# Kernel tuning notes

Measured on AMD Instinct MI355X. Metric: run time of the kernel, lower is better.

Reference implementation:

```python
import jax, jax.numpy as jnp
import numpy as np

N, F_IN, HEADS, D_HEAD, HID, OUT, E = 50000, 128, 4, 64, 256, 2, 800000
NEG_SLOPE = 0.2


def setup_inputs() -> dict:
    key = jax.random.key(0)
    ks = jax.random.split(key, 12)
    x = jax.random.normal(ks[0], (N, F_IN), dtype=jnp.float32)
    edge_index = jax.random.randint(ks[1], (2, E), 0, N, dtype=jnp.int64)
    s = 0.05
    W_gat = jax.random.normal(ks[2], (F_IN, HEADS * D_HEAD), dtype=jnp.float32) * s
    att_src = jax.random.normal(ks[3], (HEADS, D_HEAD), dtype=jnp.float32) * s
    att_dst = jax.random.normal(ks[4], (HEADS, D_HEAD), dtype=jnp.float32) * s
    b_gat = jnp.zeros((HEADS * D_HEAD,), dtype=jnp.float32)
    W1 = jax.random.normal(ks[5], (HEADS * D_HEAD, HID), dtype=jnp.float32) * s
    b1 = jnp.zeros((HID,), dtype=jnp.float32)
    W2 = jax.random.normal(ks[6], (HID, HID), dtype=jnp.float32) * s
    b2 = jnp.zeros((HID,), dtype=jnp.float32)
    W3 = jax.random.normal(ks[7], (HID, OUT), dtype=jnp.float32) * s
    b3 = jnp.zeros((OUT,), dtype=jnp.float32)
    return {"x": x, "edge_index": edge_index, "W_gat": W_gat, "att_src": att_src,
            "att_dst": att_dst, "b_gat": b_gat, "W1": W1, "b1": b1,
            "W2": W2, "b2": b2, "W3": W3, "b3": b3}


def _gat(x, edge_index, W_gat, att_src, att_dst, b_gat):
    n = x.shape[0]
    loop = jnp.arange(n, dtype=edge_index.dtype)
    src = jnp.concatenate([edge_index[0], loop])  # [E+N] message sources j
    dst = jnp.concatenate([edge_index[1], loop])  # [E+N] message targets i
    h = (x @ W_gat).reshape(n, HEADS, D_HEAD)      # [N,H,D]
    a_s = jnp.einsum('nhd,hd->nh', h, att_src)     # [N,H]
    a_d = jnp.einsum('nhd,hd->nh', h, att_dst)     # [N,H]
    e = a_s[src] + a_d[dst]                        # [E',H]
    e = jax.nn.leaky_relu(e, NEG_SLOPE)
    # per-destination-node softmax over incoming edges (numerically stable)
    emax = jax.ops.segment_max(e, dst, num_segments=n)
    e = jnp.exp(e - emax[dst])
    denom = jax.ops.segment_sum(e, dst, num_segments=n)
    alpha = e / denom[dst]                         # [E',H]
    msg = h[src] * alpha[:, :, None]               # [E',H,D]
    out = jax.ops.segment_sum(msg, dst, num_segments=n)  # [N,H,D]
    return out.reshape(n, HEADS * D_HEAD) + b_gat


def reference(x, edge_index, W_gat, att_src, att_dst, b_gat, W1, b1, W2, b2, W3, b3):
    h = _gat(x, edge_index, W_gat, att_src, att_dst, b_gat)
    h = jax.nn.relu(h @ W1 + b1)
    h = jax.nn.relu(h @ W2 + b2)
    return h @ W3 + b3
```

## Files before the change

### kernel.cpp

```cpp
#include <hip/hip_runtime.h>
#include <math.h>

#define N_NODES 50000
#define NP 50048
#define F_IN 128
#define HD 256
#define HID 256
#define NE 800000
#define CAP 64
#define NEG_SLOPE 0.2f

#define G1_BLOCKS (NP / 64)
#define FILL_BLOCKS (NE / 256)
#define TR_BLOCKS 32

typedef __attribute__((ext_vector_type(8))) __bf16 bf16x8;
typedef __attribute__((ext_vector_type(4))) __bf16 bf16x4;
typedef __attribute__((ext_vector_type(4))) float f32x4;
typedef __attribute__((ext_vector_type(2))) float f32x2;

#define GLD_LDS16(g, l)                                                      \
    __builtin_amdgcn_global_load_lds(                                        \
        (const __attribute__((address_space(1))) unsigned int*)(g),          \
        (__attribute__((address_space(3))) unsigned int*)(l), 16, 0, 0)

__device__ __forceinline__ void tile_transpose(const float* __restrict__ W,
                                               __bf16* __restrict__ Wt,
                                               int K, int M, int k0, int m0,
                                               int t, float* tile) {
#pragma unroll
    for (int i = 0; i < 4; ++i) {
        int row = i * 16 + (t >> 4);
        int col = (t & 15) * 4;
        float4 v = *(const float4*)&W[(size_t)(k0 + row) * M + m0 + col];
        tile[row * 65 + col] = v.x; tile[row * 65 + col + 1] = v.y;
        tile[row * 65 + col + 2] = v.z; tile[row * 65 + col + 3] = v.w;
    }
    __syncthreads();
#pragma unroll
    for (int i = 0; i < 4; ++i) {
        int mrow = i * 16 + (t >> 4);
        int kcol = (t & 15) * 4;
        bf16x4 o = {(__bf16)tile[kcol * 65 + mrow], (__bf16)tile[(kcol + 1) * 65 + mrow],
                    (__bf16)tile[(kcol + 2) * 65 + mrow], (__bf16)tile[(kcol + 3) * 65 + mrow]};
        *(bf16x4*)&Wt[(size_t)(m0 + mrow) * K + k0 + kcol] = o;
    }
}

__global__ __launch_bounds__(256) void prep_kernel(const float* __restrict__ Wg,
                                                   __bf16* __restrict__ Wg_t) {
    __shared__ float tile[64 * 65];
    int b = blockIdx.x, t = threadIdx.x;
    tile_transpose(Wg, Wg_t, F_IN, HD, (b >> 2) * 64, (b & 3) * 64, t, tile);
}

__global__ __launch_bounds__(256) void g1_fill_kernel(const float* __restrict__ x,
                                                      const __bf16* __restrict__ Bt,
                                                      const float* __restrict__ att_src,
                                                      const float* __restrict__ att_dst,
                                                      const int* __restrict__ ew,
                                                      __bf16* __restrict__ h,
                                                      float* __restrict__ a_s,
                                                      float* __restrict__ a_d,
                                                      int* __restrict__ cnt,
                                                      unsigned short* __restrict__ bucket,
                                                      const float* __restrict__ W1,
                                                      const float* __restrict__ W2,
                                                      __bf16* __restrict__ W1_t,
                                                      __bf16* __restrict__ W2_t) {
    __shared__ __align__(16) char smem[20480];
    __bf16* As = (__bf16*)smem;
    __bf16* Bs = (__bf16*)(smem + 4096);

    if (blockIdx.x >= G1_BLOCKS + FILL_BLOCKS) {
        int b = blockIdx.x - G1_BLOCKS - FILL_BLOCKS;
        float* tile = (float*)smem;
        if (b < 16)
            tile_transpose(W1, W1_t, HD, HID, (b >> 2) * 64, (b & 3) * 64,
                           threadIdx.x, tile);
        else {
            b -= 16;
            tile_transpose(W2, W2_t, HID, HID, (b >> 2) * 64, (b & 3) * 64,
                           threadIdx.x, tile);
        }
        return;
    }
    if (blockIdx.x >= G1_BLOCKS) {
        int e = (blockIdx.x - G1_BLOCKS) * 256 + threadIdx.x;
        int hi = ew[2 * e + 1];
        unsigned long long bal = __ballot(hi != 0);
        int src, dst;
        if (bal == 0) { src = ew[2 * e]; dst = ew[2 * NE + 2 * e]; }
        else          { src = ew[e];     dst = ew[NE + e]; }
        int pos = atomicAdd(&cnt[dst], 1);
        if (pos < CAP - 1)
            bucket[dst * CAP + pos] = (unsigned short)src;
        return;
    }

    const int t = threadIdx.x;
    const int lane = t & 63, wv = t >> 6;
    const int lr = lane & 15, q = lane >> 4, lk = q * 8;
    const int col_off = wv * 64;
    const int row0 = blockIdx.x * 64;
    const int sr = t >> 2, sk = (t & 3) * 8;
    const int arow = row0 + sr;
    const bool avalid = arow < N_NODES;

    f32x4 acc[4][4];
#pragma unroll
    for (int r = 0; r < 4; ++r)
#pragma unroll
        for (int c = 0; c < 4; ++c) acc[r][c] = f32x4{0.f, 0.f, 0.f, 0.f};

    for (int k0 = 0; k0 < F_IN; k0 += 32) {
        float4 v0 = {0, 0, 0, 0}, v1 = {0, 0, 0, 0};
        if (avalid) {
            const float* xp = &x[(size_t)arow * F_IN + k0 + sk];
            v0 = *(const float4*)xp;
            v1 = *(const float4*)(xp + 4);
        }
        bf16x8 o;
        o[0] = (__bf16)v0.x; o[1] = (__bf16)v0.y; o[2] = (__bf16)v0.z; o[3] = (__bf16)v0.w;
        o[4] = (__bf16)v1.x; o[5] = (__bf16)v1.y; o[6] = (__bf16)v1.z; o[7] = (__bf16)v1.w;
        *(bf16x8*)&As[sr * 32 + sk] = o;
#pragma unroll
        for (int s = 0; s < 4; ++s) {
            int r = s * 64 + sr;
            GLD_LDS16(&Bt[(size_t)r * F_IN + k0 + sk], &Bs[r * 32 + sk]);
        }
        __syncthreads();
        bf16x8 af[4], bfr[4];
#pragma unroll
        for (int i = 0; i < 4; ++i) {
            af[i]  = *(const bf16x8*)&As[(i * 16 + lr) * 32 + lk];
            bfr[i] = *(const bf16x8*)&Bs[(col_off + i * 16 + lr) * 32 + lk];
        }
#pragma unroll
        for (int r = 0; r < 4; ++r)
#pragma unroll
            for (int c = 0; c < 4; ++c)
                acc[r][c] = __builtin_amdgcn_mfma_f32_16x16x32_bf16(af[r], bfr[c], acc[r][c], 0, 0, 0);
        __syncthreads();
    }

    float asv[4], adv[4];
#pragma unroll
    for (int c = 0; c < 4; ++c) {
        int col = col_off + c * 16 + lr;
        asv[c] = att_src[col];
        adv[c] = att_dst[col];
    }
    float ps[4][4], pd[4][4];
#pragma unroll
    for (int r = 0; r < 4; ++r)
#pragma unroll
        for (int i = 0; i < 4; ++i) { ps[r][i] = 0.f; pd[r][i] = 0.f; }

#pragma unroll
    for (int c = 0; c < 4; ++c) {
        int col = col_off + c * 16 + lr;
#pragma unroll
        for (int r = 0; r < 4; ++r) {
#pragma unroll
            for (int i = 0; i < 4; ++i) {
                int row = row0 + r * 16 + q * 4 + i;
                float v = acc[r][c][i];
                h[(size_t)row * HD + col] = (__bf16)v;
                ps[r][i] += v * asv[c];
                pd[r][i] += v * adv[c];
            }
        }
    }
#pragma unroll
    for (int r = 0; r < 4; ++r)
#pragma unroll
        for (int i = 0; i < 4; ++i) {
#pragma unroll
            for (int m = 1; m < 16; m <<= 1) {
                ps[r][i] += __shfl_xor(ps[r][i], m);
                pd[r][i] += __shfl_xor(pd[r][i], m);
            }
        }
    if (lr == 0) {
#pragma unroll
        for (int r = 0; r < 4; ++r)
#pragma unroll
            for (int i = 0; i < 4; ++i) {
                int row = row0 + r * 16 + q * 4 + i;
                a_s[row * 4 + wv] = ps[r][i];
                a_d[row * 4 + wv] = pd[r][i];
            }
    }
}

__device__ __forceinline__ float lrelu(float v) { return v >= 0.f ? v : NEG_SLOPE * v; }

__device__ __forceinline__ f32x2 bf2f(unsigned u) {
    f32x2 r;
    r.x = __uint_as_float(u << 16);
    r.y = __uint_as_float(u & 0xffff0000u);
    return r;
}

__global__ __launch_bounds__(128) void gat_aggregate_kernel(const __bf16* __restrict__ h,
                                                            const float* __restrict__ a_s,
                                                            const float* __restrict__ a_d,
                                                            const int* __restrict__ cnt,
                                                            const unsigned short* __restrict__ bucket,
                                                            const float* __restrict__ b_gat,
                                                            __bf16* __restrict__ gat) {
    __shared__ unsigned short s_src[2][64];
    __shared__ float s_alpha[2][64][4];
    const int lane = threadIdx.x & 63;
    const int wv = threadIdx.x >> 6;
    const int n = blockIdx.x * 2 + wv;

    int deg_e = cnt[n];
    if (deg_e > CAP - 1) deg_e = CAP - 1;
    const int deg = deg_e + 1;
    int src = n;
    float4 wgt = {0, 0, 0, 0};
    float4 ad = *(const float4*)&a_d[n * 4];
    if (lane < deg) {
        if (lane < deg_e) src = bucket[n * CAP + lane];
        float4 as4 = *(const float4*)&a_s[src * 4];
        wgt.x = __expf(lrelu(as4.x + ad.x));
        wgt.y = __expf(lrelu(as4.y + ad.y));
        wgt.z = __expf(lrelu(as4.z + ad.z));
        wgt.w = __expf(lrelu(as4.w + ad.w));
    }
    float4 s = wgt;
#pragma unroll
    for (int off = 1; off < 64; off <<= 1) {
        s.x += __shfl_xor(s.x, off); s.y += __shfl_xor(s.y, off);
        s.z += __shfl_xor(s.z, off); s.w += __shfl_xor(s.w, off);
    }
    s_src[wv][lane] = (unsigned short)src;
    s_alpha[wv][lane][0] = wgt.x / s.x;
    s_alpha[wv][lane][1] = wgt.y / s.y;
    s_alpha[wv][lane][2] = wgt.z / s.z;
    s_alpha[wv][lane][3] = wgt.w / s.w;

    const int half = lane >> 5;
    const int l32 = lane & 31;
    const int c0 = l32 * 8;
    const int head = l32 >> 3;
    f32x2 acc2[4];
#pragma unroll
    for (int k = 0; k < 4; ++k) acc2[k] = f32x2{0.f, 0.f};

    const int mde = (deg + 1) & ~1;
    int j = 0;
    for (; j + 8 <= mde; j += 8) {
        int j0 = j + half, j1 = j + 2 + half, j2 = j + 4 + half, j3 = j + 6 + half;
        int s0 = s_src[wv][j0], s1 = s_src[wv][j1];
        int s2 = s_src[wv][j2], s3 = s_src[wv][j3];
        f32x2 a0 = {s_alpha[wv][j0][head], s_alpha[wv][j0][head]};
        f32x2 a1 = {s_alpha[wv][j1][head], s_alpha[wv][j1][head]};
        f32x2 a2 = {s_alpha[wv][j2][head], s_alpha[wv][j2][head]};
        f32x2 a3 = {s_alpha[wv][j3][head], s_alpha[wv][j3][head]};
        uint4 u0 = *(const uint4*)&h[(size_t)s0 * HD + c0];
        uint4 u1 = *(const uint4*)&h[(size_t)s1 * HD + c0];
        uint4 u2 = *(const uint4*)&h[(size_t)s2 * HD + c0];
        uint4 u3 = *(const uint4*)&h[(size_t)s3 * HD + c0];
        acc2[0] += a0 * bf2f(u0.x) + a1 * bf2f(u1.x) + a2 * bf2f(u2.x) + a3 * bf2f(u3.x);
        acc2[1] += a0 * bf2f(u0.y) + a1 * bf2f(u1.y) + a2 * bf2f(u2.y) + a3 * bf2f(u3.y);
        acc2[2] += a0 * bf2f(u0.z) + a1 * bf2f(u1.z) + a2 * bf2f(u2.z) + a3 * bf2f(u3.z);
        acc2[3] += a0 * bf2f(u0.w) + a1 * bf2f(u1.w) + a2 * bf2f(u2.w) + a3 * bf2f(u3.w);
    }
    for (; j < mde; j += 2) {
        int j0 = j + half;
        int s0 = s_src[wv][j0];
        f32x2 a0 = {s_alpha[wv][j0][head], s_alpha[wv][j0][head]};
        uint4 u0 = *(const uint4*)&h[(size_t)s0 * HD + c0];
        acc2[0] += a0 * bf2f(u0.x);
        acc2[1] += a0 * bf2f(u0.y);
        acc2[2] += a0 * bf2f(u0.z);
        acc2[3] += a0 * bf2f(u0.w);
    }
#pragma unroll
    for (int k = 0; k < 4; ++k) {
        acc2[k].x += __shfl_xor(acc2[k].x, 32);
        acc2[k].y += __shfl_xor(acc2[k].y, 32);
    }

    if (half == 0) {
        float4 bg0 = *(const float4*)&b_gat[c0];
        float4 bg1 = *(const float4*)&b_gat[c0 + 4];
        bf16x8 o;
        o[0] = (__bf16)(acc2[0].x + bg0.x); o[1] = (__bf16)(acc2[0].y + bg0.y);
        o[2] = (__bf16)(acc2[1].x + bg0.z); o[3] = (__bf16)(acc2[1].y + bg0.w);
        o[4] = (__bf16)(acc2[2].x + bg1.x); o[5] = (__bf16)(acc2[2].y + bg1.y);
        o[6] = (__bf16)(acc2[3].x + bg1.z); o[7] = (__bf16)(acc2[3].y + bg1.w);
        *(bf16x8*)&gat[(size_t)n * HD + c0] = o;
    }
}

__global__ __launch_bounds__(256) void fused_mlp_kernel(const __bf16* __restrict__ A,
                                                        const __bf16* __restrict__ W1t,
                                                        const __bf16* __restrict__ W2t,
                                                        const float* __restrict__ b1,
                                                        const float* __restrict__ b2,
                                                        const float* __restrict__ W3,
                                                        const float* __restrict__ b3,
                                                        float* __restrict__ out) {
    __shared__ __bf16 As[64 * 32];
    __shared__ __bf16 Ws[256 * 32];
    __shared__ __bf16 h1s[8 * 64 * 32];
    __shared__ float s_out[64][2];
    const int t = threadIdx.x;
    const int lane = t & 63, wv = t >> 6;
    const int lr = lane & 15, q = lane >> 4, lk = q * 8;
    const int col_off = wv * 64;
    const int row0 = blockIdx.x * 64;
    const int sr = t >> 2, sk = (t & 3) * 8;

    if (t < 128) ((float*)s_out)[t] = 0.f;

    f32x4 acc[4][4];
#pragma unroll
    for (int r = 0; r < 4; ++r)
#pragma unroll
        for (int c = 0; c < 4; ++c) acc[r][c] = f32x4{0.f, 0.f, 0.f, 0.f};

    for (int k0 = 0; k0 < HD; k0 += 32) {
        GLD_LDS16(&A[(size_t)(row0 + sr) * HD + k0 + sk], &As[sr * 32 + sk]);
#pragma unroll
        for (int s = 0; s < 4; ++s) {
            int r = s * 64 + sr;
            GLD_LDS16(&W1t[(size_t)r * HD + k0 + sk], &Ws[r * 32 + sk]);
        }
        __syncthreads();
        bf16x8 af[4], bfr[4];
#pragma unroll
        for (int i = 0; i < 4; ++i) {
            af[i]  = *(const bf16x8*)&As[(i * 16 + lr) * 32 + lk];
            bfr[i] = *(const bf16x8*)&Ws[(col_off + i * 16 + lr) * 32 + lk];
        }
#pragma unroll
        for (int r = 0; r < 4; ++r)
#pragma unroll
            for (int c = 0; c < 4; ++c)
                acc[r][c] = __builtin_amdgcn_mfma_f32_16x16x32_bf16(af[r], bfr[c], acc[r][c], 0, 0, 0);
        __syncthreads();
    }
#pragma unroll
    for (int c = 0; c < 4; ++c) {
        int col = col_off + c * 16 + lr;
        float bv = b1[col];
        int cb = (col >> 5) * 2048;
        int kk = col & 31;
#pragma unroll
        for (int r = 0; r < 4; ++r)
#pragma unroll
            for (int i = 0; i < 4; ++i) {
                int row = r * 16 + q * 4 + i;
                float v = fmaxf(acc[r][c][i] + bv, 0.f);
                h1s[cb + row * 32 + kk] = (__bf16)v;
                acc[r][c][i] = 0.f;
            }
    }
    __syncthreads();

    for (int k0 = 0; k0 < HID; k0 += 32) {
#pragma unroll
        for (int s = 0; s < 4; ++s) {
            int r = s * 64 + sr;
            GLD_LDS16(&W2t[(size_t)r * HID + k0 + sk], &Ws[r * 32 + sk]);
        }
        __syncthreads();
        const int cb = (k0 >> 5) * 2048;
        bf16x8 af[4], bfr[4];
#pragma unroll
        for (int i = 0; i < 4; ++i) {
            af[i]  = *(const bf16x8*)&h1s[cb + (i * 16 + lr) * 32 + lk];
            bfr[i] = *(const bf16x8*)&Ws[(col_off + i * 16 + lr) * 32 + lk];
        }
#pragma unroll
        for (int r = 0; r < 4; ++r)
#pragma unroll
            for (int c = 0; c < 4; ++c)
                acc[r][c] = __builtin_amdgcn_mfma_f32_16x16x32_bf16(af[r], bfr[c], acc[r][c], 0, 0, 0);
        __syncthreads();
    }

    float b2v[4], w30[4], w31[4];
#pragma unroll
    for (int c = 0; c < 4; ++c) {
        int col = col_off + c * 16 + lr;
        b2v[c] = b2[col];
        w30[c] = W3[col * 2];
        w31[c] = W3[col * 2 + 1];
    }
#pragma unroll
    for (int r = 0; r < 4; ++r) {
#pragma unroll
        for (int i = 0; i < 4; ++i) {
            float o0 = 0.f, o1 = 0.f;
#pragma unroll
            for (int c = 0; c < 4; ++c) {
                float v = fmaxf(acc[r][c][i] + b2v[c], 0.f);
                o0 += v * w30[c];
                o1 += v * w31[c];
            }
#pragma unroll
            for (int m = 1; m < 16; m <<= 1) {
                o0 += __shfl_xor(o0, m);
                o1 += __shfl_xor(o1, m);
            }
            if (lr == 0) {
                int row = r * 16 + q * 4 + i;
                atomicAdd(&s_out[row][0], o0);
                atomicAdd(&s_out[row][1], o1);
            }
        }
    }
    __syncthreads();
    if (t < 128) {
        int row = t >> 1, o = t & 1;
        int g = row0 + row;
        if (g < N_NODES) out[g * 2 + o] = s_out[row][o] + b3[o];
    }
}

extern "C" void kernel_launch(void* const* d_in, const int* in_sizes, int n_in,
                              void* d_out, int out_size, void* d_ws, size_t ws_size,
                              hipStream_t stream) {
    const float* x       = (const float*)d_in[0];
    const int*   ei      = (const int*)d_in[1];
    const float* W_gat   = (const float*)d_in[2];
    const float* att_src = (const float*)d_in[3];
    const float* att_dst = (const float*)d_in[4];
    const float* b_gat   = (const float*)d_in[5];
    const float* W1      = (const float*)d_in[6];
    const float* b1      = (const float*)d_in[7];
    const float* W2      = (const float*)d_in[8];
    const float* b2      = (const float*)d_in[9];
    const float* W3      = (const float*)d_in[10];
    const float* b3      = (const float*)d_in[11];
    float* out = (float*)d_out;

    char* ws = (char*)d_ws;
    __bf16* h_bf   = (__bf16*)ws;  ws += (size_t)NP * HD * 2;
    __bf16* gat_bf = (__bf16*)ws;  ws += (size_t)NP * HD * 2;
    __bf16* Wg_t   = (__bf16*)ws;  ws += (size_t)HD * F_IN * 2;
    __bf16* W1_t   = (__bf16*)ws;  ws += (size_t)HID * HD * 2;
    __bf16* W2_t   = (__bf16*)ws;  ws += (size_t)HID * HID * 2;
    float* a_s     = (float*)ws;   ws += (size_t)NP * 4 * 4;
    float* a_d     = (float*)ws;   ws += (size_t)NP * 4 * 4;
    int* cnt       = (int*)ws;     ws += (size_t)N_NODES * 4;
    unsigned short* bucket = (unsigned short*)ws;
    ws += (size_t)N_NODES * CAP * 2;

    hipMemsetAsync(cnt, 0, (size_t)N_NODES * 4, stream);
    prep_kernel<<<8, 256, 0, stream>>>(W_gat, Wg_t);
    g1_fill_kernel<<<G1_BLOCKS + FILL_BLOCKS + TR_BLOCKS, 256, 0, stream>>>(
        x, Wg_t, att_src, att_dst, ei, h_bf, a_s, a_d, cnt, bucket,
        W1, W2, W1_t, W2_t);
    gat_aggregate_kernel<<<N_NODES / 2, 128, 0, stream>>>(h_bf, a_s, a_d, cnt, bucket,
                                                          b_gat, gat_bf);
    fused_mlp_kernel<<<NP / 64, 256, 0, stream>>>(gat_bf, W1_t, W2_t, b1, b2, W3, b3, out);
}
```

Before: 243.8 us.

## Split fused MLP into two GEMM kernels and fold cnt memset into prep

Removes the hipMemsetAsync by zeroing the bucket counters with extra blocks of the prep kernel, saving one launch. Splits the fused two-layer MLP into two templated GEMM launches. The first writes the ReLU hidden layer to a global bf16 buffer, and the second computes layer 2 plus the W3 projection. This drops the 32KB LDS staging of h1 so more blocks may fit per CU, at the cost of an extra global round trip for h1 (about 25MB written and read) and one more kernel launch.

```diff
diff --git a/kernel.cpp b/kernel.cpp
--- a/kernel.cpp
+++ b/kernel.cpp
@@ -48,10 +48,16 @@
 }
 
 __global__ __launch_bounds__(256) void prep_kernel(const float* __restrict__ Wg,
-                                                   __bf16* __restrict__ Wg_t) {
+                                                   __bf16* __restrict__ Wg_t,
+                                                   int* __restrict__ cnt) {
     __shared__ float tile[64 * 65];
     int b = blockIdx.x, t = threadIdx.x;
-    tile_transpose(Wg, Wg_t, F_IN, HD, (b >> 2) * 64, (b & 3) * 64, t, tile);
+    if (b < 8) {
+        tile_transpose(Wg, Wg_t, F_IN, HD, (b >> 2) * 64, (b & 3) * 64, t, tile);
+    } else {
+        int i4 = (b - 8) * 256 + t;
+        if (i4 < (N_NODES + 3) / 4) ((int4*)cnt)[i4] = int4{0, 0, 0, 0};
+    }
 }
 
 __global__ __launch_bounds__(256) void g1_fill_kernel(const float* __restrict__ x,
@@ -297,17 +303,16 @@
     }
 }
 
-__global__ __launch_bounds__(256) void fused_mlp_kernel(const __bf16* __restrict__ A,
-                                                        const __bf16* __restrict__ W1t,
-                                                        const __bf16* __restrict__ W2t,
-                                                        const float* __restrict__ b1,
-                                                        const float* __restrict__ b2,
-                                                        const float* __restrict__ W3,
-                                                        const float* __restrict__ b3,
-                                                        float* __restrict__ out) {
+template <bool FINAL>
+__global__ __launch_bounds__(256) void gemm_kernel(const __bf16* __restrict__ A,
+                                                   const __bf16* __restrict__ Bt,
+                                                   const float* __restrict__ bias,
+                                                   __bf16* __restrict__ C,
+                                                   const float* __restrict__ W3,
+                                                   const float* __restrict__ b3,
+                                                   float* __restrict__ out) {
     __shared__ __bf16 As[64 * 32];
-    __shared__ __bf16 Ws[256 * 32];
-    __shared__ __bf16 h1s[8 * 64 * 32];
+    __shared__ __bf16 Bs[256 * 32];
     __shared__ float s_out[64][2];
     const int t = threadIdx.x;
     const int lane = t & 63, wv = t >> 6;
@@ -316,7 +321,7 @@
     const int row0 = blockIdx.x * 64;
     const int sr = t >> 2, sk = (t & 3) * 8;
 
-    if (t < 128) ((float*)s_out)[t] = 0.f;
+    if (FINAL && t < 128) ((float*)s_out)[t] = 0.f;
 
     f32x4 acc[4][4];
 #pragma unroll
@@ -324,19 +329,19 @@
 #pragma unroll
         for (int c = 0; c < 4; ++c) acc[r][c] = f32x4{0.f, 0.f, 0.f, 0.f};
 
-    for (int k0 = 0; k0 < HD; k0 += 32) {
-        GLD_LDS16(&A[(size_t)(row0 + sr) * HD + k0 + sk], &As[sr * 32 + sk]);
+    for (int k0 = 0; k0 < 256; k0 += 32) {
+        GLD_LDS16(&A[(size_t)(row0 + sr) * 256 + k0 + sk], &As[sr * 32 + sk]);
 #pragma unroll
         for (int s = 0; s < 4; ++s) {
             int r = s * 64 + sr;
-            GLD_LDS16(&W1t[(size_t)r * HD + k0 + sk], &Ws[r * 32 + sk]);
+            GLD_LDS16(&Bt[(size_t)r * 256 + k0 + sk], &Bs[r * 32 + sk]);
         }
         __syncthreads();
         bf16x8 af[4], bfr[4];
 #pragma unroll
         for (int i = 0; i < 4; ++i) {
             af[i]  = *(const bf16x8*)&As[(i * 16 + lr) * 32 + lk];
-            bfr[i] = *(const bf16x8*)&Ws[(col_off + i * 16 + lr) * 32 + lk];
+            bfr[i] = *(const bf16x8*)&Bs[(col_off + i * 16 + lr) * 32 + lk];
         }
 #pragma unroll
         for (int r = 0; r < 4; ++r)
@@ -345,82 +350,58 @@
                 acc[r][c] = __builtin_amdgcn_mfma_f32_16x16x32_bf16(af[r], bfr[c], acc[r][c], 0, 0, 0);
         __syncthreads();
     }
-#pragma unroll
-    for (int c = 0; c < 4; ++c) {
-        int col = col_off + c * 16 + lr;
-        float bv = b1[col];
-        int cb = (col >> 5) * 2048;
-        int kk = col & 31;
-#pragma unroll
-        for (int r = 0; r < 4; ++r)
+
+    if constexpr (!FINAL) {
+#pragma unroll
+        for (int c = 0; c < 4; ++c) {
+            int col = col_off + c * 16 + lr;
+            float bv = bias[col];
+#pragma unroll
+            for (int r = 0; r < 4; ++r)
+#pragma unroll
+                for (int i = 0; i < 4; ++i) {
+                    int row = row0 + r * 16 + q * 4 + i;
+                    C[(size_t)row * 256 + col] = (__bf16)fmaxf(acc[r][c][i] + bv, 0.f);
+                }
+        }
+    } else {
+        float b2v[4], w30[4], w31[4];
+#pragma unroll
+        for (int c = 0; c < 4; ++c) {
+            int col = col_off + c * 16 + lr;
+            b2v[c] = bias[col];
+            w30[c] = W3[col * 2];
+            w31[c] = W3[col * 2 + 1];
+        }
+#pragma unroll
+        for (int r = 0; r < 4; ++r) {
 #pragma unroll
             for (int i = 0; i < 4; ++i) {
-                int row = r * 16 + q * 4 + i;
-                float v = fmaxf(acc[r][c][i] + bv, 0.f);
-                h1s[cb + row * 32 + kk] = (__bf16)v;
-                acc[r][c][i] = 0.f;
+                float o0 = 0.f, o1 = 0.f;
+#pragma unroll
+                for (int c = 0; c < 4; ++c) {
+                    float v = fmaxf(acc[r][c][i] + b2v[c], 0.f);
+                    o0 += v * w30[c];
+                    o1 += v * w31[c];
+                }
+#pragma unroll
+                for (int m = 1; m < 16; m <<= 1) {
+                    o0 += __shfl_xor(o0, m);
+                    o1 += __shfl_xor(o1, m);
+                }
+                if (lr == 0) {
+                    int row = r * 16 + q * 4 + i;
+                    atomicAdd(&s_out[row][0], o0);
+                    atomicAdd(&s_out[row][1], o1);
+                }
             }
-    }
-    __syncthreads();
-
-    for (int k0 = 0; k0 < HID; k0 += 32) {
-#pragma unroll
-        for (int s = 0; s < 4; ++s) {
-            int r = s * 64 + sr;
-            GLD_LDS16(&W2t[(size_t)r * HID + k0 + sk], &Ws[r * 32 + sk]);
         }
         __syncthreads();
-        const int cb = (k0 >> 5) * 2048;
-        bf16x8 af[4], bfr[4];
-#pragma unroll
-        for (int i = 0; i < 4; ++i) {
-            af[i]  = *(const bf16x8*)&h1s[cb + (i * 16 + lr) * 32 + lk];
-            bfr[i] = *(const bf16x8*)&Ws[(col_off + i * 16 + lr) * 32 + lk];
-        }
-#pragma unroll
-        for (int r = 0; r < 4; ++r)
-#pragma unroll
-            for (int c = 0; c < 4; ++c)
-                acc[r][c] = __builtin_amdgcn_mfma_f32_16x16x32_bf16(af[r], bfr[c], acc[r][c], 0, 0, 0);
-        __syncthreads();
-    }
-
-    float b2v[4], w30[4], w31[4];
-#pragma unroll
-    for (int c = 0; c < 4; ++c) {
-        int col = col_off + c * 16 + lr;
-        b2v[c] = b2[col];
-        w30[c] = W3[col * 2];
-        w31[c] = W3[col * 2 + 1];
-    }
-#pragma unroll
-    for (int r = 0; r < 4; ++r) {
-#pragma unroll
-        for (int i = 0; i < 4; ++i) {
-            float o0 = 0.f, o1 = 0.f;
-#pragma unroll
-            for (int c = 0; c < 4; ++c) {
-                float v = fmaxf(acc[r][c][i] + b2v[c], 0.f);
-                o0 += v * w30[c];
-                o1 += v * w31[c];
-            }
-#pragma unroll
-            for (int m = 1; m < 16; m <<= 1) {
-                o0 += __shfl_xor(o0, m);
-                o1 += __shfl_xor(o1, m);
-            }
-            if (lr == 0) {
-                int row = r * 16 + q * 4 + i;
-                atomicAdd(&s_out[row][0], o0);
-                atomicAdd(&s_out[row][1], o1);
-            }
-        }
-    }
-    __syncthreads();
-    if (t < 128) {
-        int row = t >> 1, o = t & 1;
-        int g = row0 + row;
-        if (g < N_NODES) out[g * 2 + o] = s_out[row][o] + b3[o];
+        if (t < 128) {
+            int row = t >> 1, o = t & 1;
+            int g = row0 + row;
+            if (g < N_NODES) out[g * 2 + o] = s_out[row][o] + b3[o];
+        }
     }
 }
 
@@ -444,6 +425,7 @@
     char* ws = (char*)d_ws;
     __bf16* h_bf   = (__bf16*)ws;  ws += (size_t)NP * HD * 2;
     __bf16* gat_bf = (__bf16*)ws;  ws += (size_t)NP * HD * 2;
+    __bf16* h1_bf  = (__bf16*)ws;  ws += (size_t)NP * HID * 2;
     __bf16* Wg_t   = (__bf16*)ws;  ws += (size_t)HD * F_IN * 2;
     __bf16* W1_t   = (__bf16*)ws;  ws += (size_t)HID * HD * 2;
     __bf16* W2_t   = (__bf16*)ws;  ws += (size_t)HID * HID * 2;
@@ -453,12 +435,14 @@
     unsigned short* bucket = (unsigned short*)ws;
     ws += (size_t)N_NODES * CAP * 2;
 
-    hipMemsetAsync(cnt, 0, (size_t)N_NODES * 4, stream);
-    prep_kernel<<<8, 256, 0, stream>>>(W_gat, Wg_t);
+    prep_kernel<<<8 + 49, 256, 0, stream>>>(W_gat, Wg_t, cnt);
     g1_fill_kernel<<<G1_BLOCKS + FILL_BLOCKS + TR_BLOCKS, 256, 0, stream>>>(
         x, Wg_t, att_src, att_dst, ei, h_bf, a_s, a_d, cnt, bucket,
         W1, W2, W1_t, W2_t);
     gat_aggregate_kernel<<<N_NODES / 2, 128, 0, stream>>>(h_bf, a_s, a_d, cnt, bucket,
                                                           b_gat, gat_bf);
-    fused_mlp_kernel<<<NP / 64, 256, 0, stream>>>(gat_bf, W1_t, W2_t, b1, b2, W3, b3, out);
-}
+    gemm_kernel<false><<<NP / 64, 256, 0, stream>>>(gat_bf, W1_t, b1, h1_bf,
+                                                    nullptr, nullptr, nullptr);
+    gemm_kernel<true><<<NP / 64, 256, 0, stream>>>(h1_bf, W2_t, b2, nullptr,
+                                                   W3, b3, out);
+}
```

Result: slower. 254.4 us (+4.3%).
